# Kernel tuning notes

Hardware: AMD Instinct MI355X
Metric: run time of the kernel (lower is better)

## Reference

```python
import jax, jax.numpy as jnp
import numpy as np

B, IN, H, O, T = 4096, 128, 1024, 64, 25  # batch, static feat, hidden, outputs, steps


def setup_inputs() -> dict:
    key = jax.random.key(0)
    ks = jax.random.split(key, 11)
    s = 1.0 / np.sqrt(H)  # PyTorch LSTM/Linear uniform init scale
    u = lambda k, sh: jax.random.uniform(k, sh, jnp.float32, -s, s)
    return {
        "static_input": jax.random.normal(ks[0], (B, IN), jnp.float32),
        "W_ih0": u(ks[1], (4 * H, IN + O)),
        "W_hh0": u(ks[2], (4 * H, H)),
        "b_ih0": u(ks[3], (4 * H,)),
        "b_hh0": u(ks[4], (4 * H,)),
        "W_ih1": u(ks[5], (4 * H, H)),
        "W_hh1": u(ks[6], (4 * H, H)),
        "b_ih1": u(ks[7], (4 * H,)),
        "b_hh1": u(ks[8], (4 * H,)),
        "W_out": u(ks[9], (O, H)),
        "b_out": u(ks[10], (O,)),
        "num_steps": T,
    }


def _lstm_cell(x, h, c, W_ih, W_hh, b):
    # PyTorch gate order: input, forget, cell(g), output
    g = x @ W_ih.T + h @ W_hh.T + b
    i, f, gg, o = jnp.split(g, 4, axis=-1)
    c_new = jax.nn.sigmoid(f) * c + jax.nn.sigmoid(i) * jnp.tanh(gg)
    h_new = jax.nn.sigmoid(o) * jnp.tanh(c_new)
    return h_new, c_new


def reference(static_input, W_ih0, W_hh0, b_ih0, b_hh0,
              W_ih1, W_hh1, b_ih1, b_hh1, W_out, b_out, num_steps):
    b0 = b_ih0 + b_hh0
    b1 = b_ih1 + b_hh1
    batch = static_input.shape[0]
    hid = W_hh0.shape[1]
    out_dim = W_out.shape[0]
    z = jnp.zeros((batch, hid), jnp.float32)
    y0 = jnp.zeros((batch, out_dim), jnp.float32)  # output_seq[:, 0] is zeros at t=0

    def step(carry, _):
        h1, c1, h2, c2, y_prev = carry
        x = jnp.concatenate([static_input, y_prev], axis=-1)  # [B, IN+O]
        h1, c1 = _lstm_cell(x, h1, c1, W_ih0, W_hh0, b0)
        h2, c2 = _lstm_cell(h1, h2, c2, W_ih1, W_hh1, b1)
        y = h2 @ W_out.T + b_out  # [B, O]
        return (h1, c1, h2, c2, y), y

    _, ys = jax.lax.scan(step, (z, z, z, z, y0), None, length=num_steps)
    return jnp.transpose(ys, (1, 0, 2))  # [B, T, O]
```

## Files before the change

kernel.cpp:

```cpp
#include <hip/hip_runtime.h>

#define BATCH  4096
#define HID    1024
#define NOUT   64
#define TSTEPS 25
#define KA2    1280
#define KA2R   1216
#define KB     2048
#define LDY    1600

typedef __attribute__((ext_vector_type(8))) __bf16 bf16x8;
typedef __attribute__((ext_vector_type(4))) float  floatx4;

__device__ __forceinline__ unsigned short f2bf(float f) {
    union { float f; unsigned u; } v; v.f = f;
    unsigned r = v.u + 0x7fffu + ((v.u >> 16) & 1u);
    return (unsigned short)(r >> 16);
}
__device__ __forceinline__ float rcpf(float x) { return __builtin_amdgcn_rcpf(x); }
__device__ __forceinline__ float sigmf(float x) { return rcpf(1.0f + __expf(-x)); }
__device__ __forceinline__ float tanh_fast(float x) {
    float ax = fabsf(x);
    float e  = __expf(-2.0f * ax);
    float t  = (1.0f - e) * rcpf(1.0f + e);
    return copysignf(t, x);
}

#define GLDS16(gp, lp) __builtin_amdgcn_global_load_lds( \
    (const __attribute__((address_space(1))) void*)(gp), \
    (__attribute__((address_space(3))) void*)(lp), 16, 0, 0)

#define SB() __builtin_amdgcn_sched_barrier(0)

__global__ __launch_bounds__(512, 2) void lstm_gate_gemm(
    const unsigned short* __restrict__ X, int K,
    const unsigned short* __restrict__ W,
    const float* __restrict__ ginit,
    float* __restrict__ cell,
    unsigned short* __restrict__ d1, int ld1, int off1,
    unsigned short* __restrict__ d2, int ld2, int off2,
    float* __restrict__ dfp)
{
    __shared__ __align__(16) char smem[131072];

    const int tid  = threadIdx.x;
    const int lane = tid & 63;
    const int w    = tid >> 6;
    const int ql   = lane >> 4;
    const int lr   = lane & 15;
    const int wr   = w >> 2;
    const int wc   = w & 3;

    const int id  = blockIdx.y * 16 + blockIdx.x;
    const int xcd = id & 7;
    const int c   = id >> 3;
    const int bx  = (xcd & 3) * 4 + (c & 3);
    const int by  = (xcd >> 2) * 8 + (c >> 2);
    const int m0  = bx * 256;
    const int j0  = by * 64;

    const int s0  = w * 128 + lane;
    const int r0  = s0 >> 3;
    const int kc0 = (s0 & 7) ^ (r0 & 7);
    const unsigned sOff = (unsigned)s0 * 16;
    const unsigned short* sA[2];
    const unsigned short* sB[2];
    sA[0] = X + (size_t)(m0 + r0) * K + kc0 * 8;
    sA[1] = X + (size_t)(m0 + 128 + r0) * K + kc0 * 8;
    {
        const int nb0 = r0, nb1 = 128 + r0;
        sB[0] = W + (size_t)((nb0 & 3) * HID + j0 + (nb0 >> 2)) * K + kc0 * 8;
        sB[1] = W + (size_t)((nb1 & 3) * HID + j0 + (nb1 >> 2)) * K + kc0 * 8;
    }

#define STAGE_A(h, tt, p) do { \
    const unsigned short* _s = sA[h] + (size_t)(tt) * 64; \
    char* _d = smem + (p) + (h) * 16384 + sOff; \
    GLDS16(_s, _d); \
    GLDS16(_s + 8 * (size_t)K, _d + 1024); \
} while (0)

#define STAGE_B(h, tt, p) do { \
    const unsigned short* _s = sB[h] + (size_t)(tt) * 64; \
    char* _d = smem + (p) + 32768 + (h) * 16384 + sOff; \
    GLDS16(_s, _d); \
    GLDS16(_s + 2 * (size_t)K, _d + 1024); \
} while (0)

    unsigned offA[4], offB[2];
#pragma unroll
    for (int fi = 0; fi < 4; ++fi) {
        int r = wr * 64 + fi * 16 + lr;
        offA[fi] = (unsigned)((r * 8 + (ql ^ (r & 7))) * 16);
    }
#pragma unroll
    for (int fj = 0; fj < 2; ++fj) {
        int r = wc * 32 + fj * 16 + lr;
        offB[fj] = (unsigned)(32768 + (r * 8 + (ql ^ (r & 7))) * 16);
    }

#define LOAD_A(AV, BASE) do { \
    const char* _ab = smem + (BASE); \
    _Pragma("unroll") \
    for (int fi = 0; fi < 4; ++fi) { \
        AV[fi][0] = *(const bf16x8*)(_ab + offA[fi]); \
        AV[fi][1] = *(const bf16x8*)(_ab + (offA[fi] ^ 64u)); \
    } \
} while (0)

#define LOAD_B(BV, BASE) do { \
    const char* _bb = smem + (BASE); \
    _Pragma("unroll") \
    for (int fj = 0; fj < 2; ++fj) { \
        BV[fj][0] = *(const bf16x8*)(_bb + offB[fj]); \
        BV[fj][1] = *(const bf16x8*)(_bb + (offB[fj] ^ 64u)); \
    } \
} while (0)

#define MFMA_PART(Q, AV, BV, F0, F1) do { \
    __builtin_amdgcn_s_setprio(1); \
    _Pragma("unroll") \
    for (int fi = (F0); fi < (F1); ++fi) \
    _Pragma("unroll") \
    for (int fj = 0; fj < 2; ++fj) \
    _Pragma("unroll") \
    for (int kk = 0; kk < 2; ++kk) \
        acc[Q][fi][fj] = __builtin_amdgcn_mfma_f32_16x16x32_bf16( \
            AV[fi][kk], BV[fj][kk], acc[Q][fi][fj], 0, 0, 0); \
    __builtin_amdgcn_s_setprio(0); \
} while (0)

    floatx4 acc[4][4][2];
#pragma unroll
    for (int q = 0; q < 4; ++q)
#pragma unroll
        for (int i = 0; i < 4; ++i)
#pragma unroll
            for (int j = 0; j < 2; ++j)
                acc[q][i][j] = floatx4{0.f, 0.f, 0.f, 0.f};

    const int NT = K >> 6;

    bf16x8 av0[4][2], av1[4][2], bv0[2][2], bv1[2][2];

    STAGE_B(1, 0, 0); STAGE_A(1, 0, 0); STAGE_A(0, 0, 0); STAGE_B(0, 0, 0);
    STAGE_B(1, 1, 65536); STAGE_A(1, 1, 65536); STAGE_A(0, 1, 65536); STAGE_B(0, 1, 65536);
    asm volatile("s_waitcnt vmcnt(8)");
    __builtin_amdgcn_s_barrier();
    SB();
    LOAD_A(av0, 0);
    LOAD_B(bv0, 0);
    LOAD_B(bv1, 16384);
    SB();

    int par = 0;
    for (int t = 0; t < NT; ++t) {
        const int cur = par << 16;
        const int np  = cur ^ 65536;
        const int t2  = (t + 2 < NT) ? t + 2 : NT - 1;
        __builtin_amdgcn_s_barrier();
        SB();
        MFMA_PART(0, av0, bv0, 0, 1);
        SB();
        LOAD_A(av1, cur + 16384);
        STAGE_B(1, t2, cur);
        SB();
        MFMA_PART(0, av0, bv0, 1, 4);
        SB();
        __builtin_amdgcn_s_barrier();
        SB();
        MFMA_PART(1, av0, bv1, 0, 1);
        SB();
        STAGE_A(1, t2, cur);
        SB();
        MFMA_PART(1, av0, bv1, 1, 4);
        SB();
        asm volatile("s_waitcnt vmcnt(6)");
        __builtin_amdgcn_s_barrier();
        SB();
        MFMA_PART(2, av1, bv1, 0, 1);
        SB();
        LOAD_A(av0, np);
        STAGE_A(0, t2, cur);
        SB();
        MFMA_PART(2, av1, bv1, 1, 4);
        SB();
        asm volatile("s_waitcnt vmcnt(6)");
        __builtin_amdgcn_s_barrier();
        SB();
        MFMA_PART(3, av1, bv0, 0, 1);
        SB();
        LOAD_B(bv1, np + 16384);
        STAGE_B(0, t2, cur);
        SB();
        MFMA_PART(3, av1, bv0, 1, 4);
        SB();
        LOAD_B(bv0, np);
        par ^= 1;
    }

    asm volatile("s_waitcnt vmcnt(0)");
    __builtin_amdgcn_s_barrier();

    float* scratch = (float*)(void*)smem + w * 640;
    const int jj   = lane & 7;
    const int rsel = lane >> 3;

    float  cpre[4][4][2];
    float4 gi4[4];
#pragma unroll
    for (int qd = 0; qd < 4; ++qd) {
        const int qa = (qd >= 2) ? 1 : 0;
        const int qb = (qd == 1 || qd == 2) ? 1 : 0;
        const int rowbase = m0 + qa * 128 + wr * 64;
        const int jg = j0 + qb * 32 + wc * 8 + jj;
        gi4[qd] = *(const float4*)(ginit + (size_t)jg * 4);
#pragma unroll
        for (int fi = 0; fi < 4; ++fi)
#pragma unroll
            for (int p = 0; p < 2; ++p)
                cpre[qd][fi][p] = cell[(size_t)(rowbase + fi * 16 + rsel + p * 8) * HID + jg];
    }

#pragma unroll
    for (int qd = 0; qd < 4; ++qd) {
        const int qa = (qd >= 2) ? 1 : 0;
        const int qb = (qd == 1 || qd == 2) ? 1 : 0;
        const int rowbase = m0 + qa * 128 + wr * 64;
        const int jg = j0 + qb * 32 + wc * 8 + jj;
        const float4 gi = gi4[qd];
#pragma unroll
        for (int fi = 0; fi < 4; ++fi) {
#pragma unroll
            for (int fj = 0; fj < 2; ++fj)
#pragma unroll
                for (int r = 0; r < 4; ++r)
                    scratch[(ql * 4 + r) * 36 + fj * 16 + lr] = acc[qd][fi][fj][r];
            asm volatile("" ::: "memory");
#pragma unroll
            for (int p = 0; p < 2; ++p) {
                const int row = rsel + p * 8;
                const float4 g = *(const float4*)(scratch + row * 36 + jj * 4);
                const int b = rowbase + fi * 16 + row;
                float iv = sigmf(g.x + gi.x);
                float fv = sigmf(g.y + gi.y);
                float gv = tanh_fast(g.z + gi.z);
                float ov = sigmf(g.w + gi.w);
                size_t ci = (size_t)b * HID + jg;
                float cn = fv * cpre[qd][fi][p] + iv * gv;
                cell[ci] = cn;
                float hv = ov * tanh_fast(cn);
                unsigned short hb = f2bf(hv);
                d1[(size_t)b * ld1 + off1 + jg] = hb;
                if (d2)  d2[(size_t)b * ld2 + off2 + jg] = hb;
                if (dfp) dfp[(size_t)b * HID + jg] = hv;
            }
            asm volatile("" ::: "memory");
        }
    }
#undef MFMA_PART
#undef LOAD_A
#undef LOAD_B
#undef STAGE_A
#undef STAGE_B
}

__global__ __launch_bounds__(256) void out_gemm(
    const float* __restrict__ h2, const float* __restrict__ wt,
    const float* __restrict__ bout, float* __restrict__ y,
    unsigned short* __restrict__ xn)
{
    __shared__ float hl[16 * 1024];
    const int tid = threadIdx.x;
    const int b0 = blockIdx.x * 16;
#pragma unroll
    for (int r = 0; r < 16; ++r) {
        int f4 = r * 256 + tid;
        *(float4*)(hl + f4 * 4) = *(const float4*)(h2 + (size_t)b0 * 1024 + f4 * 4);
    }
    __syncthreads();
    const int o  = tid & 63;
    const int wv = tid >> 6;
    float a0 = 0.f, a1 = 0.f, a2 = 0.f, a3 = 0.f;
#pragma unroll 8
    for (int k = 0; k < 1024; ++k) {
        float wvv = wt[k * 64 + o];
        const float* hr = hl + (wv * 4) * 1024 + k;
        a0 += hr[0]    * wvv;
        a1 += hr[1024] * wvv;
        a2 += hr[2048] * wvv;
        a3 += hr[3072] * wvv;
    }
    float bo = bout[o];
    int b = b0 + wv * 4;
    float yv[4] = {a0 + bo, a1 + bo, a2 + bo, a3 + bo};
#pragma unroll
    for (int r = 0; r < 4; ++r) {
        y[(size_t)(b + r) * LDY + o] = yv[r];
        xn[(size_t)(b + r) * KA2 + o] = f2bf(yv[r]);
    }
}

__global__ void build_woutT(const float* __restrict__ wout, float* __restrict__ wt)
{
    int idx = blockIdx.x * 256 + threadIdx.x;
    int o = idx & 63, k = idx >> 6;
    wt[idx] = wout[(size_t)o * 1024 + k];
}

__global__ void build_bias(const float* __restrict__ a, const float* __restrict__ b,
                           float* __restrict__ o)
{
    int idx = blockIdx.x * 256 + threadIdx.x;
    int gate = idx & 3, j = idx >> 2;
    int n = gate * 1024 + j;
    o[idx] = a[n] + b[n];
}

__global__ __launch_bounds__(256) void build_w0(
    const float* __restrict__ wih, const float* __restrict__ whh,
    unsigned short* __restrict__ w0)
{
    int idx = blockIdx.x * 256 + threadIdx.x;
    int n = idx / 320;
    int c = (idx - n * 320) * 4;
    float4 v = {0.f, 0.f, 0.f, 0.f};
    if (c < 64)        v = *(const float4*)(wih + (size_t)n * 192 + 128 + c);
    else if (c < 192)  v = *(const float4*)(wih + (size_t)n * 192 + (c - 64));
    else if (c < 1216) v = *(const float4*)(whh + (size_t)n * 1024 + (c - 192));
    ushort4 o;
    o.x = f2bf(v.x); o.y = f2bf(v.y); o.z = f2bf(v.z); o.w = f2bf(v.w);
    *(ushort4*)(w0 + (size_t)n * KA2 + c) = o;
}

__global__ __launch_bounds__(256) void build_w1(
    const float* __restrict__ wih, const float* __restrict__ whh,
    unsigned short* __restrict__ w1)
{
    int idx = blockIdx.x * 256 + threadIdx.x;
    int n = idx >> 9;
    int c = (idx & 511) * 4;
    float4 v;
    if (c < 1024) v = *(const float4*)(wih + (size_t)n * 1024 + c);
    else          v = *(const float4*)(whh + (size_t)n * 1024 + (c - 1024));
    ushort4 o;
    o.x = f2bf(v.x); o.y = f2bf(v.y); o.z = f2bf(v.z); o.w = f2bf(v.w);
    *(ushort4*)(w1 + (size_t)n * KB + c) = o;
}

__global__ __launch_bounds__(256) void build_x0static(
    const float* __restrict__ stat, unsigned short* __restrict__ xa,
    unsigned short* __restrict__ xb)
{
    int idx = blockIdx.x * 256 + threadIdx.x;
    int b = idx >> 5;
    int c = (idx & 31) * 4;
    float4 v = *(const float4*)(stat + (size_t)b * 128 + c);
    ushort4 o;
    o.x = f2bf(v.x); o.y = f2bf(v.y); o.z = f2bf(v.z); o.w = f2bf(v.w);
    *(ushort4*)(xa + (size_t)b * KA2 + 64 + c) = o;
    *(ushort4*)(xb + (size_t)b * KA2 + 64 + c) = o;
}

extern "C" void kernel_launch(void* const* d_in, const int* in_sizes, int n_in,
                              void* d_out, int out_size, void* d_ws, size_t ws_size,
                              hipStream_t stream)
{
    (void)in_sizes; (void)n_in; (void)out_size; (void)ws_size;
    const float* static_in = (const float*)d_in[0];
    const float* Wih0 = (const float*)d_in[1];
    const float* Whh0 = (const float*)d_in[2];
    const float* bih0 = (const float*)d_in[3];
    const float* bhh0 = (const float*)d_in[4];
    const float* Wih1 = (const float*)d_in[5];
    const float* Whh1 = (const float*)d_in[6];
    const float* bih1 = (const float*)d_in[7];
    const float* bhh1 = (const float*)d_in[8];
    const float* Wout = (const float*)d_in[9];
    const float* bout = (const float*)d_in[10];
    float* out = (float*)d_out;

    char* p = (char*)d_ws;
    size_t off = 0;
    auto take = [&](size_t n) { char* r = p + off; off += (n + 255) & ~(size_t)255; return r; };

    unsigned short* W0   = (unsigned short*)take((size_t)4096 * KA2 * 2);
    unsigned short* W1   = (unsigned short*)take((size_t)4096 * KB * 2);
    float*          B1b  = (float*)take(4096 * 4);
    float*          B0b  = (float*)take(4096 * 4);
    float*          WoT  = (float*)take((size_t)1024 * 64 * 4);
    float*          H2f  = (float*)take((size_t)BATCH * HID * 4);
    float*          C1   = (float*)take((size_t)BATCH * HID * 4);
    float*          C2   = (float*)take((size_t)BATCH * HID * 4);
    unsigned short* X0a  = (unsigned short*)take((size_t)BATCH * KA2 * 2);
    unsigned short* X0b  = (unsigned short*)take((size_t)BATCH * KA2 * 2);
    unsigned short* X1a  = (unsigned short*)take((size_t)BATCH * KB * 2);
    unsigned short* X1b  = (unsigned short*)take((size_t)BATCH * KB * 2);

    hipMemsetAsync(C1, 0, (size_t)BATCH * HID * 4, stream);
    hipMemsetAsync(C2, 0, (size_t)BATCH * HID * 4, stream);
    hipMemsetAsync(X0a, 0, (size_t)BATCH * KA2 * 2, stream);
    hipMemsetAsync(X0b, 0, (size_t)BATCH * KA2 * 2, stream);
    hipMemsetAsync(X1a, 0, (size_t)BATCH * KB * 2, stream);

    build_w0<<<5120, 256, 0, stream>>>(Wih0, Whh0, W0);
    build_w1<<<8192, 256, 0, stream>>>(Wih1, Whh1, W1);
    build_woutT<<<256, 256, 0, stream>>>(Wout, WoT);
    build_bias<<<16, 256, 0, stream>>>(bih0, bhh0, B0b);
    build_bias<<<16, 256, 0, stream>>>(bih1, bhh1, B1b);
    build_x0static<<<512, 256, 0, stream>>>(static_in, X0a, X0b);

    dim3 grid(16, 16);
    for (int t = 0; t < TSTEPS; ++t) {
        unsigned short* X0c = (t & 1) ? X0b : X0a;
        unsigned short* X0n = (t & 1) ? X0a : X0b;
        unsigned short* X1c = (t & 1) ? X1b : X1a;
        unsigned short* X1n = (t & 1) ? X1a : X1b;
        lstm_gate_gemm<<<grid, 512, 0, stream>>>(X0c, KA2, W0, B0b, C1,
                                                 X1c, KB, 0, X0n, KA2, 192, nullptr);
        lstm_gate_gemm<<<grid, 512, 0, stream>>>(X1c, KB, W1, B1b, C2,
                                                 X1n, KB, 1024, nullptr, 0, 0, H2f);
        out_gemm<<<256, 256, 0, stream>>>(H2f, WoT, bout, out + t * NOUT, X0n);
    }
}
```

Baseline: 3.655 ms.

## Load weight operand directly from global into registers, halving LDS footprint

The gate GEMM now fetches the W (B operand) fragments straight from global memory into registers, one k-tile ahead, instead of staging them through LDS. Only the activation tile goes through LDS, so shared memory per block drops from 128 KiB to 64 KiB and the main loop is rebuilt as a two-tile unrolled schedule with fewer barriers. The trade is more register pressure and uncoalesced 16-byte global loads per lane for the weights. Each wave also now re-reads weight data that was previously shared across waves through LDS. The smaller LDS footprint could allow better occupancy.

```diff
diff --git a/kernel.cpp b/kernel.cpp
--- a/kernel.cpp
+++ b/kernel.cpp
@@ -5,7 +5,6 @@
 #define NOUT   64
 #define TSTEPS 25
 #define KA2    1280
-#define KA2R   1216
 #define KB     2048
 #define LDY    1600
 
@@ -41,7 +40,7 @@
     unsigned short* __restrict__ d2, int ld2, int off2,
     float* __restrict__ dfp)
 {
-    __shared__ __align__(16) char smem[131072];
+    __shared__ __align__(16) char smem[65536];
 
     const int tid  = threadIdx.x;
     const int lane = tid & 63;
@@ -64,14 +63,8 @@
     const int kc0 = (s0 & 7) ^ (r0 & 7);
     const unsigned sOff = (unsigned)s0 * 16;
     const unsigned short* sA[2];
-    const unsigned short* sB[2];
     sA[0] = X + (size_t)(m0 + r0) * K + kc0 * 8;
     sA[1] = X + (size_t)(m0 + 128 + r0) * K + kc0 * 8;
-    {
-        const int nb0 = r0, nb1 = 128 + r0;
-        sB[0] = W + (size_t)((nb0 & 3) * HID + j0 + (nb0 >> 2)) * K + kc0 * 8;
-        sB[1] = W + (size_t)((nb1 & 3) * HID + j0 + (nb1 >> 2)) * K + kc0 * 8;
-    }
 
 #define STAGE_A(h, tt, p) do { \
     const unsigned short* _s = sA[h] + (size_t)(tt) * 64; \
@@ -80,53 +73,52 @@
     GLDS16(_s + 8 * (size_t)K, _d + 1024); \
 } while (0)
 
-#define STAGE_B(h, tt, p) do { \
-    const unsigned short* _s = sB[h] + (size_t)(tt) * 64; \
-    char* _d = smem + (p) + 32768 + (h) * 16384 + sOff; \
-    GLDS16(_s, _d); \
-    GLDS16(_s + 2 * (size_t)K, _d + 1024); \
-} while (0)
-
-    unsigned offA[4], offB[2];
+    unsigned offA[4];
 #pragma unroll
     for (int fi = 0; fi < 4; ++fi) {
         int r = wr * 64 + fi * 16 + lr;
         offA[fi] = (unsigned)((r * 8 + (ql ^ (r & 7))) * 16);
     }
-#pragma unroll
-    for (int fj = 0; fj < 2; ++fj) {
-        int r = wc * 32 + fj * 16 + lr;
-        offB[fj] = (unsigned)(32768 + (r * 8 + (ql ^ (r & 7))) * 16);
-    }
-
-#define LOAD_A(AV, BASE) do { \
-    const char* _ab = smem + (BASE); \
-    _Pragma("unroll") \
-    for (int fi = 0; fi < 4; ++fi) { \
-        AV[fi][0] = *(const bf16x8*)(_ab + offA[fi]); \
-        AV[fi][1] = *(const bf16x8*)(_ab + (offA[fi] ^ 64u)); \
+
+    const unsigned short* bp[4];
+#pragma unroll
+    for (int i = 0; i < 4; ++i) {
+        int nb = (i >> 1) * 128 + wc * 32 + (i & 1) * 16 + lr;
+        int rowg = (nb & 3) * HID + j0 + (nb >> 2);
+        bp[i] = W + (size_t)rowg * K + ql * 8;
+    }
+
+#define LOADP(DST, BOFF, FP) do { \
+    const char* _p = smem + (BOFF); \
+    _Pragma("unroll") \
+    for (int fi2 = 0; fi2 < 2; ++fi2) { \
+        DST[fi2][0] = *(const bf16x8*)(_p + offA[(FP) * 2 + fi2]); \
+        DST[fi2][1] = *(const bf16x8*)(_p + (offA[(FP) * 2 + fi2] ^ 64u)); \
     } \
 } while (0)
 
-#define LOAD_B(BV, BASE) do { \
-    const char* _bb = smem + (BASE); \
-    _Pragma("unroll") \
-    for (int fj = 0; fj < 2; ++fj) { \
-        BV[fj][0] = *(const bf16x8*)(_bb + offB[fj]); \
-        BV[fj][1] = *(const bf16x8*)(_bb + (offB[fj] ^ 64u)); \
-    } \
+#define BL4(BN, BH, TN) do { \
+    _Pragma("unroll") \
+    for (int fj = 0; fj < 2; ++fj) \
+    _Pragma("unroll") \
+    for (int kk = 0; kk < 2; ++kk) \
+        BN[BH][fj][kk] = *(const bf16x8*)(bp[(BH) * 2 + fj] + (size_t)(TN) * 64 + kk * 32); \
 } while (0)
 
-#define MFMA_PART(Q, AV, BV, F0, F1) do { \
+#define MFMAP(H, FP, AS, BS) do { \
     __builtin_amdgcn_s_setprio(1); \
     _Pragma("unroll") \
-    for (int fi = (F0); fi < (F1); ++fi) \
+    for (int fi2 = 0; fi2 < 2; ++fi2) \
+    _Pragma("unroll") \
+    for (int bh = 0; bh < 2; ++bh) \
     _Pragma("unroll") \
     for (int fj = 0; fj < 2; ++fj) \
     _Pragma("unroll") \
     for (int kk = 0; kk < 2; ++kk) \
-        acc[Q][fi][fj] = __builtin_amdgcn_mfma_f32_16x16x32_bf16( \
-            AV[fi][kk], BV[fj][kk], acc[Q][fi][fj], 0, 0, 0); \
+        acc[(H) ? (3 - bh) : bh][(FP) * 2 + fi2][fj] = \
+            __builtin_amdgcn_mfma_f32_16x16x32_bf16( \
+                AS[fi2][kk], BS[bh][fj][kk], \
+                acc[(H) ? (3 - bh) : bh][(FP) * 2 + fi2][fj], 0, 0, 0); \
     __builtin_amdgcn_s_setprio(0); \
 } while (0)
 
@@ -141,62 +133,55 @@
 
     const int NT = K >> 6;
 
-    bf16x8 av0[4][2], av1[4][2], bv0[2][2], bv1[2][2];
-
-    STAGE_B(1, 0, 0); STAGE_A(1, 0, 0); STAGE_A(0, 0, 0); STAGE_B(0, 0, 0);
-    STAGE_B(1, 1, 65536); STAGE_A(1, 1, 65536); STAGE_A(0, 1, 65536); STAGE_B(0, 1, 65536);
-    asm volatile("s_waitcnt vmcnt(8)");
+    bf16x8 aA[2][2], aB[2][2];
+    bf16x8 bA[2][2][2], bB[2][2][2];
+
+    SB();
+    STAGE_A(0, 0, 0); STAGE_A(1, 0, 0);
+    SB();
+    BL4(bA, 0, 0); BL4(bA, 1, 0);
+    SB();
+    STAGE_A(0, 1, 32768); STAGE_A(1, 1, 32768);
+    SB();
+    asm volatile("s_waitcnt vmcnt(12)");
     __builtin_amdgcn_s_barrier();
     SB();
-    LOAD_A(av0, 0);
-    LOAD_B(bv0, 0);
-    LOAD_B(bv1, 16384);
-    SB();
-
-    int par = 0;
-    for (int t = 0; t < NT; ++t) {
-        const int cur = par << 16;
-        const int np  = cur ^ 65536;
-        const int t2  = (t + 2 < NT) ? t + 2 : NT - 1;
-        __builtin_amdgcn_s_barrier();
-        SB();
-        MFMA_PART(0, av0, bv0, 0, 1);
-        SB();
-        LOAD_A(av1, cur + 16384);
-        STAGE_B(1, t2, cur);
-        SB();
-        MFMA_PART(0, av0, bv0, 1, 4);
-        SB();
-        __builtin_amdgcn_s_barrier();
-        SB();
-        MFMA_PART(1, av0, bv1, 0, 1);
-        SB();
-        STAGE_A(1, t2, cur);
-        SB();
-        MFMA_PART(1, av0, bv1, 1, 4);
-        SB();
-        asm volatile("s_waitcnt vmcnt(6)");
-        __builtin_amdgcn_s_barrier();
-        SB();
-        MFMA_PART(2, av1, bv1, 0, 1);
-        SB();
-        LOAD_A(av0, np);
-        STAGE_A(0, t2, cur);
-        SB();
-        MFMA_PART(2, av1, bv1, 1, 4);
-        SB();
-        asm volatile("s_waitcnt vmcnt(6)");
-        __builtin_amdgcn_s_barrier();
-        SB();
-        MFMA_PART(3, av1, bv0, 0, 1);
-        SB();
-        LOAD_B(bv1, np + 16384);
-        STAGE_B(0, t2, cur);
-        SB();
-        MFMA_PART(3, av1, bv0, 1, 4);
-        SB();
-        LOAD_B(bv0, np);
-        par ^= 1;
+    LOADP(aA, 0, 0);
+    SB();
+
+#define TILE(TT, BUF, NBUF, BC, BN) do { \
+    const int t2 = ((TT) + 2 < NT) ? (TT) + 2 : NT - 1; \
+    const int tn = ((TT) + 1 < NT) ? (TT) + 1 : NT - 1; \
+     \
+    SB(); \
+    LOADP(aB, (BUF), 1); \
+    SB(); \
+    MFMAP(0, 0, aA, BC); \
+     \
+    SB(); \
+    LOADP(aA, (BUF) + 16384, 0); \
+    BL4(BN, 0, tn); \
+    SB(); \
+    MFMAP(0, 1, aB, BC); \
+     \
+    SB(); \
+    LOADP(aB, (BUF) + 16384, 1); \
+    BL4(BN, 1, tn); \
+    SB(); \
+    MFMAP(1, 0, aA, BC); \
+     \
+    asm volatile("s_waitcnt vmcnt(8)"); \
+    __builtin_amdgcn_s_barrier(); \
+    SB(); \
+    LOADP(aA, (NBUF), 0); \
+    STAGE_A(0, t2, (BUF)); STAGE_A(1, t2, (BUF)); \
+    SB(); \
+    MFMAP(1, 1, aB, BC); \
+} while (0)
+
+    for (int t = 0; t < NT; t += 2) {
+        TILE(t,     0,     32768, bA, bB);
+        TILE(t + 1, 32768, 0,     bB, bA);
     }
 
     asm volatile("s_waitcnt vmcnt(0)");
@@ -258,11 +243,11 @@
             asm volatile("" ::: "memory");
         }
     }
-#undef MFMA_PART
-#undef LOAD_A
-#undef LOAD_B
+#undef TILE
+#undef MFMAP
+#undef BL4
+#undef LOADP
 #undef STAGE_A
-#undef STAGE_B
 }
 
 __global__ __launch_bounds__(256) void out_gemm(
```

New measurement: 4.888 ms. 1.34x slower.
